# Kernel optimization log

Hardware: AMD Instinct MI355X
Metric: run time of the kernel (lower is better)

Reference implementation:

```python
import jax, jax.numpy as jnp
import numpy as np

N = 16384
E = 524288
IN_DIM = 512
HID = 256
NCLS = 64


def setup_inputs() -> dict:
    key = jax.random.key(0)
    k1, k2, k3, k4, k5, k6 = jax.random.split(key, 6)
    X = jax.random.normal(k1, (N, IN_DIM), dtype=jnp.float32)
    edge_index = jax.random.randint(k2, (2, E), 0, N, dtype=jnp.int64)
    # torch nn.Linear params: y = x @ W.T + b
    W1 = jax.random.normal(k3, (HID, IN_DIM), dtype=jnp.float32) * (1.0 / np.sqrt(IN_DIM))
    b1 = jax.random.normal(k4, (HID,), dtype=jnp.float32) * 0.01
    W2 = jax.random.normal(k5, (NCLS, HID), dtype=jnp.float32) * (1.0 / np.sqrt(HID))
    b2 = jax.random.normal(k6, (NCLS,), dtype=jnp.float32) * 0.01
    return {"X": X, "edge_index": edge_index, "W1": W1, "b1": b1, "W2": W2, "b2": b2}


def _build_a_hat(edge_index, n):
    # Dense adjacency via scatter-set, exactly as the torch code does.
    A = jnp.zeros((n, n), dtype=jnp.float32)
    A = A.at[edge_index[0], edge_index[1]].set(1.0)
    A = A + A.T
    A = (A > 0).astype(jnp.float32)
    A = A + jnp.eye(n, dtype=jnp.float32)
    # symmetric normalization: D^-1/2 A D^-1/2 (diag matmuls == broadcast)
    deg = A.sum(axis=1)
    dis = jnp.power(deg + 1e-8, -0.5)
    return dis[:, None] * A * dis[None, :]


def reference(X, edge_index, W1, b1, W2, b2):
    n = X.shape[0]
    A_hat = _build_a_hat(edge_index, n)
    H = A_hat @ X                      # [N, in_dim]
    H = H @ W1.T + b1                  # lin1
    H = jax.nn.relu(H)
    # dropout is identity in eval mode
    H = A_hat @ H                      # [N, hidden]
    H = H @ W2.T + b2                  # lin2 -> [N, num_classes]
    return H
```

## Files before the change

kernel.cpp:

```cpp
#include <hip/hip_runtime.h>
#include <stdint.h>

#define N_NODES 16384
#define N_EDGES 524288
#define IN_DIM  512
#define HID     256
#define NCLS    64
#define LSTRIDE 192
#define NBKT    1024
#define NBBLK   256
#define ENT     4096
#define OFFSTRIDE 1032
#define GEMM_BLKS 256

typedef __bf16 bf16x8 __attribute__((ext_vector_type(8)));
typedef float  f32x4  __attribute__((ext_vector_type(4)));
typedef unsigned int u32x4 __attribute__((ext_vector_type(4)));

__device__ __forceinline__ unsigned short f2bf(float f) {
    unsigned int u = __float_as_uint(f);
    u += 0x7FFFu + ((u >> 16) & 1u);
    return (unsigned short)(u >> 16);
}
__device__ __forceinline__ float bflo(unsigned int u) { return __uint_as_float(u << 16); }
__device__ __forceinline__ float bfhi(unsigned int u) { return __uint_as_float(u & 0xFFFF0000u); }

__device__ __forceinline__ void fma8(float* a, uint4 u, float w) {
    a[0] = fmaf(w, bflo(u.x), a[0]); a[1] = fmaf(w, bfhi(u.x), a[1]);
    a[2] = fmaf(w, bflo(u.y), a[2]); a[3] = fmaf(w, bfhi(u.y), a[3]);
    a[4] = fmaf(w, bflo(u.z), a[4]); a[5] = fmaf(w, bfhi(u.z), a[5]);
    a[6] = fmaf(w, bflo(u.w), a[6]); a[7] = fmaf(w, bfhi(u.w), a[7]);
}
__device__ __forceinline__ void add8(float* a, uint4 u) {
    a[0] += bflo(u.x); a[1] += bfhi(u.x);
    a[2] += bflo(u.y); a[3] += bfhi(u.y);
    a[4] += bflo(u.z); a[5] += bfhi(u.z);
    a[6] += bflo(u.w); a[7] += bfhi(u.w);
}

__device__ __forceinline__ void bucket_body(
    int blk, const void* __restrict__ ep, unsigned int* __restrict__ offbuf,
    unsigned int* __restrict__ gbuf, char* smem) {
    unsigned int* lcnt   = (unsigned int*)smem;
    unsigned int* loff   = lcnt + NBKT;
    unsigned int* sorted = loff + NBKT;
    unsigned int* wsum   = sorted + ENT;
    int* sflag = (int*)(wsum + 4);
    const int tid = threadIdx.x;
    if (tid == 0) {
        const int* p = (const int*)ep;
        int odd = 1;
        for (int k = 0; k < 64; ++k)
            if (p[2 * k + 1] != 0) odd = 0;
        *sflag = odd;
    }
    #pragma unroll
    for (int q = 0; q < 4; ++q) lcnt[tid + q * 256] = 0;
    __syncthreads();

    const int e0 = blk * 2048 + tid;
    int s[8], d[8];
    if (*sflag) {
        const long long* p = (const long long*)ep;
        #pragma unroll
        for (int q = 0; q < 8; ++q) {
            s[q] = (int)p[e0 + q * 256];
            d[q] = (int)p[N_EDGES + e0 + q * 256];
        }
    } else {
        const int* p = (const int*)ep;
        #pragma unroll
        for (int q = 0; q < 8; ++q) {
            s[q] = p[e0 + q * 256];
            d[q] = p[N_EDGES + e0 + q * 256];
        }
    }
    unsigned int meta[16];
    #pragma unroll
    for (int q = 0; q < 8; ++q) {
        int b0 = s[q] >> 4, b1 = d[q] >> 4;
        unsigned int sl0 = atomicAdd(&lcnt[b0], 1u);
        unsigned int sl1 = atomicAdd(&lcnt[b1], 1u);
        meta[2 * q]     = (unsigned int)b0 | (sl0 << 10);
        meta[2 * q + 1] = (unsigned int)b1 | (sl1 << 10);
    }
    __syncthreads();

    const int lane = tid & 63, wv = tid >> 6;
    unsigned int c0 = lcnt[4 * tid], c1 = lcnt[4 * tid + 1];
    unsigned int c2 = lcnt[4 * tid + 2], c3 = lcnt[4 * tid + 3];
    unsigned int p1 = c0 + c1, p2 = p1 + c2, tot = p2 + c3;
    unsigned int inc = tot;
    #pragma unroll
    for (int dd = 1; dd < 64; dd <<= 1) {
        unsigned int v = __shfl_up(inc, dd);
        if (lane >= dd) inc += v;
    }
    if (lane == 63) wsum[wv] = inc;
    __syncthreads();
    unsigned int wbase = 0;
    #pragma unroll
    for (int w = 0; w < 3; ++w)
        if (w < wv) wbase += wsum[w];
    unsigned int base = wbase + inc - tot;
    loff[4 * tid]     = base;
    loff[4 * tid + 1] = base + c0;
    loff[4 * tid + 2] = base + p1;
    loff[4 * tid + 3] = base + p2;
    {
        uint4 ov;
        ov.x = base; ov.y = base + c0; ov.z = base + p1; ov.w = base + p2;
        *(uint4*)&offbuf[(size_t)blk * OFFSTRIDE + 4 * tid] = ov;
        if (tid == 255) offbuf[(size_t)blk * OFFSTRIDE + 1024] = ENT;
    }
    __syncthreads();

    #pragma unroll
    for (int q = 0; q < 8; ++q) {
        unsigned int m0 = meta[2 * q];
        sorted[loff[m0 & 1023u] + (m0 >> 10)] =
            ((unsigned int)(s[q] & 15) << 14) | (unsigned int)d[q];
        unsigned int m1 = meta[2 * q + 1];
        sorted[loff[m1 & 1023u] + (m1 >> 10)] =
            ((unsigned int)(d[q] & 15) << 14) | (unsigned int)s[q];
    }
    __syncthreads();

    #pragma unroll
    for (int q = 0; q < 4; ++q)
        ((uint4*)gbuf)[(size_t)blk * (ENT / 4) + tid + q * 256] =
            ((const uint4*)sorted)[tid + q * 256];
}

__global__ __launch_bounds__(256) void build_csr(
    const unsigned int* __restrict__ offbuf, const unsigned int* __restrict__ gbuf,
    float* __restrict__ dis, int* __restrict__ ncnt,
    unsigned short* __restrict__ lists) {
    __shared__ unsigned int bml[16 * 512];
    const int tid = threadIdx.x;
    const int bkt = blockIdx.x;
    const int node0 = bkt * 16;
    {
        const u32x4 z = {0, 0, 0, 0};
        #pragma unroll
        for (int q = 0; q < 8; ++q)
            ((u32x4*)bml)[tid + q * 256] = z;
    }
    __syncthreads();
    {
        const unsigned int st = offbuf[(size_t)tid * OFFSTRIDE + bkt];
        const unsigned int en = offbuf[(size_t)tid * OFFSTRIDE + bkt + 1];
        const unsigned int* sp = gbuf + (size_t)tid * ENT;
        for (unsigned int l = st; l < en; ++l) {
            unsigned int e = sp[l];
            unsigned int local = e >> 14, nbr = e & 16383u;
            atomicOr(&bml[local * 512 + (nbr >> 5)], 1u << (nbr & 31u));
        }
    }
    __syncthreads();
    const int wid = tid >> 6, lane = tid & 63;
    for (int nn = wid; nn < 16; nn += 4) {
        const int node = node0 + nn;
        const unsigned int* row = bml + nn * 512 + lane * 8;
        unsigned int w[8];
        int c = 0;
        #pragma unroll
        for (int j = 0; j < 8; ++j) { w[j] = row[j]; c += __popc(w[j]); }
        int inc = c;
        #pragma unroll
        for (int dd = 1; dd < 64; dd <<= 1) {
            int t = __shfl_up(inc, dd);
            if (lane >= dd) inc += t;
        }
        int total = __shfl(inc, 63);
        unsigned short* dst = lists + (size_t)node * LSTRIDE + (inc - c);
        int k = 0;
        #pragma unroll
        for (int j = 0; j < 8; ++j) {
            unsigned int bits = w[j];
            int base = (lane * 8 + j) * 32;
            while (bits) {
                int b = __ffs(bits) - 1;
                bits &= bits - 1;
                dst[k++] = (unsigned short)(base + b);
            }
        }
        if (lane == 63) {
            lists[(size_t)node * LSTRIDE + total] = (unsigned short)node;
            ncnt[node] = total + 1;
            dis[node] = 1.0f / sqrtf((float)(total + 1) + 1e-8f);
        }
    }
}

template <bool F32>
__device__ __forceinline__ uint4 ld_chunk(const void* __restrict__ G,
                                          size_t row, int KD, int k0, int s) {
    if constexpr (F32) {
        const float* g = (const float*)G + row * KD + k0 + s * 8;
        float4 v0 = *(const float4*)g;
        float4 v1 = *(const float4*)(g + 4);
        uint4 w;
        w.x = (unsigned int)f2bf(v0.x) | ((unsigned int)f2bf(v0.y) << 16);
        w.y = (unsigned int)f2bf(v0.z) | ((unsigned int)f2bf(v0.w) << 16);
        w.z = (unsigned int)f2bf(v1.x) | ((unsigned int)f2bf(v1.y) << 16);
        w.w = (unsigned int)f2bf(v1.z) | ((unsigned int)f2bf(v1.w) << 16);
        return w;
    } else {
        return *(const uint4*)((const unsigned short*)G + row * KD + k0 + s * 8);
    }
}

template <int BM, int BN, int KD, int ND, bool AF32, bool BF32>
__device__ __forceinline__ void gemm_body(
    int bx, int by, const void* __restrict__ Ag, const void* __restrict__ Bg,
    unsigned short* __restrict__ Cg, const float* __restrict__ dis, char* smem) {
    constexpr int FM = BM / 32, FN = BN / 32;
    constexpr int NK = KD / 64;
    unsigned short* Asm = (unsigned short*)smem;
    unsigned short* Bsm = (unsigned short*)smem + BM * 64;
    const int tid = threadIdx.x;
    const int lane = tid & 63;
    const int wid = tid >> 6;
    const int wm = wid >> 1, wn = wid & 1;
    const int m0 = bx * BM, n0 = by * BN;

    uint4 ra[BM / 32], rb[BN / 32];
    #pragma unroll
    for (int q = 0; q < BM / 32; ++q) {
        int cch = tid + 256 * q, r = cch >> 3, s = cch & 7;
        ra[q] = ld_chunk<AF32>(Ag, (size_t)(m0 + r), KD, 0, s);
    }
    #pragma unroll
    for (int q = 0; q < BN / 32; ++q) {
        int cch = tid + 256 * q, r = cch >> 3, s = cch & 7;
        rb[q] = ld_chunk<BF32>(Bg, (size_t)(n0 + r), KD, 0, s);
    }

    f32x4 acc[FM][FN] = {};

    for (int kt = 0; kt < NK; ++kt) {
        __syncthreads();
        #pragma unroll
        for (int q = 0; q < BM / 32; ++q) {
            int cch = tid + 256 * q, r = cch >> 3, s = cch & 7;
            *(uint4*)((char*)Asm + r * 128 + ((s ^ (r & 7)) << 4)) = ra[q];
        }
        #pragma unroll
        for (int q = 0; q < BN / 32; ++q) {
            int cch = tid + 256 * q, r = cch >> 3, s = cch & 7;
            *(uint4*)((char*)Bsm + r * 128 + ((s ^ (r & 7)) << 4)) = rb[q];
        }
        __syncthreads();
        if (kt + 1 < NK) {
            int k0 = (kt + 1) * 64;
            #pragma unroll
            for (int q = 0; q < BM / 32; ++q) {
                int cch = tid + 256 * q, r = cch >> 3, s = cch & 7;
                ra[q] = ld_chunk<AF32>(Ag, (size_t)(m0 + r), KD, k0, s);
            }
            #pragma unroll
            for (int q = 0; q < BN / 32; ++q) {
                int cch = tid + 256 * q, r = cch >> 3, s = cch & 7;
                rb[q] = ld_chunk<BF32>(Bg, (size_t)(n0 + r), KD, k0, s);
            }
        }
        #pragma unroll
        for (int ks = 0; ks < 2; ++ks) {
            bf16x8 af[FM], bg[FN];
            #pragma unroll
            for (int i = 0; i < FM; ++i) {
                int row = wm * (BM / 2) + i * 16 + (lane & 15);
                int slot = (ks * 4 + (lane >> 4)) ^ (row & 7);
                af[i] = *(const bf16x8*)((const char*)Asm + row * 128 + slot * 16);
            }
            #pragma unroll
            for (int j = 0; j < FN; ++j) {
                int row = wn * (BN / 2) + j * 16 + (lane & 15);
                int slot = (ks * 4 + (lane >> 4)) ^ (row & 7);
                bg[j] = *(const bf16x8*)((const char*)Bsm + row * 128 + slot * 16);
            }
            #pragma unroll
            for (int i = 0; i < FM; ++i)
                #pragma unroll
                for (int j = 0; j < FN; ++j)
                    acc[i][j] = __builtin_amdgcn_mfma_f32_16x16x32_bf16(af[i], bg[j], acc[i][j], 0, 0, 0);
        }
    }

    #pragma unroll
    for (int i = 0; i < FM; ++i) {
        #pragma unroll
        for (int e = 0; e < 4; ++e) {
            int row = m0 + wm * (BM / 2) + i * 16 + ((lane >> 4) << 2) + e;
            float dm = dis ? dis[row] : 1.0f;
            #pragma unroll
            for (int j = 0; j < FN; ++j) {
                int col = n0 + wn * (BN / 2) + j * 16 + (lane & 15);
                Cg[(size_t)row * ND + col] = f2bf(acc[i][j][e] * dm);
            }
        }
    }
}

__global__ __launch_bounds__(256) void bucket_gemm(
    const float* __restrict__ X, const float* __restrict__ W1,
    unsigned short* __restrict__ Y, const void* __restrict__ ep,
    unsigned int* __restrict__ offbuf, unsigned int* __restrict__ gbuf) {
    __shared__ __align__(16) char smem[(128 + 128) * 64 * 2];
    if (blockIdx.x < GEMM_BLKS) {
        int gb = blockIdx.x;
        gemm_body<128, 128, IN_DIM, HID, true, true>(
            gb & 127, gb >> 7, X, W1, Y, nullptr, smem);
    } else {
        bucket_body(blockIdx.x - GEMM_BLKS, ep, offbuf, gbuf, smem);
    }
}

__global__ __launch_bounds__(256) void gemm2_k(
    const unsigned short* __restrict__ H1, const float* __restrict__ W2,
    unsigned short* __restrict__ Z, const float* __restrict__ dis) {
    __shared__ __align__(16) char smem[(64 + 64) * 64 * 2];
    gemm_body<64, 64, HID, NCLS, false, true>(blockIdx.x, 0, H1, W2, Z, dis, smem);
}

__global__ __launch_bounds__(256) void spmm_hid(
    const int* __restrict__ ncnt, const unsigned short* __restrict__ lists,
    const float* __restrict__ dis, const unsigned short* __restrict__ Yp,
    const float* __restrict__ bias, unsigned short* __restrict__ H1) {
    const int bid = blockIdx.x;
    const int r = bid & 7;
    const int fh = r >> 2;
    const int wid = threadIdx.x >> 6, lane = threadIdx.x & 63;
    const int i = (bid >> 3) * 16 + (r & 3) * 4 + wid;

    __shared__ uint2 sld[4][LSTRIDE];
    const int n = min(ncnt[i], LSTRIDE);
    for (int l = lane; l < n; l += 64) {
        int j = lists[(size_t)i * LSTRIDE + l];
        uint2 m;
        m.x = __float_as_uint(dis[j]);
        m.y = (unsigned int)j << 9;
        sld[wid][l] = m;
    }

    const int qw = lane >> 4, p = lane & 15;
    const char* Ybase = (const char*)Yp + fh * 256 + p * 16;
    const uint2* slw = sld[wid];
    float acc[8] = {}, acc2[8] = {};
    int l = 0;
    const int nmain = n & ~7;
    if (nmain >= 8) {
        uint2 m0 = slw[qw];
        uint2 m1 = slw[4 + qw];
        uint4 u0 = *(const uint4*)(Ybase + m0.y);
        uint4 u1 = *(const uint4*)(Ybase + m1.y);
        float w0 = __uint_as_float(m0.x), w1 = __uint_as_float(m1.x);
        #pragma unroll 2
        for (l = 8; l < nmain; l += 8) {
            uint2 t0 = slw[l + qw];
            uint2 t1 = slw[l + 4 + qw];
            uint4 v0 = *(const uint4*)(Ybase + t0.y);
            uint4 v1 = *(const uint4*)(Ybase + t1.y);
            fma8(acc, u0, w0);
            fma8(acc2, u1, w1);
            u0 = v0; u1 = v1;
            w0 = __uint_as_float(t0.x); w1 = __uint_as_float(t1.x);
        }
        fma8(acc, u0, w0);
        fma8(acc2, u1, w1);
        l = nmain;
    }
    for (; l < n; l += 4) {
        if (l + qw < n) {
            uint2 m = slw[l + qw];
            uint4 u = *(const uint4*)(Ybase + m.y);
            fma8(acc, u, __uint_as_float(m.x));
        }
    }
    #pragma unroll
    for (int k = 0; k < 8; ++k) {
        acc[k] += acc2[k];
        acc[k] += __shfl_xor(acc[k], 16);
        acc[k] += __shfl_xor(acc[k], 32);
    }
    if (qw == 0) {
        float di = dis[i];
        float4 b0 = *(const float4*)&bias[fh * 128 + p * 8];
        float4 b1 = *(const float4*)&bias[fh * 128 + p * 8 + 4];
        float v0 = fmaxf(fmaf(di, acc[0], b0.x), 0.0f);
        float v1 = fmaxf(fmaf(di, acc[1], b0.y), 0.0f);
        float v2 = fmaxf(fmaf(di, acc[2], b0.z), 0.0f);
        float v3 = fmaxf(fmaf(di, acc[3], b0.w), 0.0f);
        float v4 = fmaxf(fmaf(di, acc[4], b1.x), 0.0f);
        float v5 = fmaxf(fmaf(di, acc[5], b1.y), 0.0f);
        float v6 = fmaxf(fmaf(di, acc[6], b1.z), 0.0f);
        float v7 = fmaxf(fmaf(di, acc[7], b1.w), 0.0f);
        u32x4 o;
        o.x = (unsigned int)f2bf(v0) | ((unsigned int)f2bf(v1) << 16);
        o.y = (unsigned int)f2bf(v2) | ((unsigned int)f2bf(v3) << 16);
        o.z = (unsigned int)f2bf(v4) | ((unsigned int)f2bf(v5) << 16);
        o.w = (unsigned int)f2bf(v6) | ((unsigned int)f2bf(v7) << 16);
        __builtin_nontemporal_store(o, (u32x4*)&H1[(size_t)i * 256 + fh * 128 + p * 8]);
    }
}

__global__ __launch_bounds__(256) void spmm_out(
    const int* __restrict__ ncnt, const unsigned short* __restrict__ lists,
    const float* __restrict__ dis, const unsigned short* __restrict__ Zp,
    const float* __restrict__ bias, float* __restrict__ out) {
    const int wid = threadIdx.x >> 6, lane = threadIdx.x & 63;
    const int i = blockIdx.x * 4 + wid;
    __shared__ unsigned int sl[4][LSTRIDE];
    const int n = min(ncnt[i], LSTRIDE);
    for (int l = lane; l < n; l += 64)
        sl[wid][l] = (unsigned int)lists[(size_t)i * LSTRIDE + l] << 7;

    const int g = lane >> 3, p = lane & 7;
    const char* Zbase = (const char*)Zp + p * 16;
    const unsigned int* slw = sl[wid];
    float acc[8] = {}, acc2[8] = {};
    int l = 0;
    const int nmain = n & ~15;
    if (nmain >= 16) {
        uint4 u0 = *(const uint4*)(Zbase + slw[g]);
        uint4 u1 = *(const uint4*)(Zbase + slw[8 + g]);
        #pragma unroll 2
        for (l = 16; l < nmain; l += 16) {
            uint4 v0 = *(const uint4*)(Zbase + slw[l + g]);
            uint4 v1 = *(const uint4*)(Zbase + slw[l + 8 + g]);
            add8(acc, u0);
            add8(acc2, u1);
            u0 = v0; u1 = v1;
        }
        add8(acc, u0);
        add8(acc2, u1);
        l = nmain;
    }
    for (; l < n; l += 8) {
        if (l + g < n) {
            uint4 u = *(const uint4*)(Zbase + slw[l + g]);
            add8(acc, u);
        }
    }
    #pragma unroll
    for (int k = 0; k < 8; ++k) {
        acc[k] += acc2[k];
        acc[k] += __shfl_xor(acc[k], 8);
        acc[k] += __shfl_xor(acc[k], 16);
        acc[k] += __shfl_xor(acc[k], 32);
    }
    if (lane < 8) {
        float di = dis[i];
        float4 b0 = *(const float4*)&bias[p * 8];
        float4 b1 = *(const float4*)&bias[p * 8 + 4];
        f32x4 o0, o1;
        o0.x = fmaf(di, acc[0], b0.x); o0.y = fmaf(di, acc[1], b0.y);
        o0.z = fmaf(di, acc[2], b0.z); o0.w = fmaf(di, acc[3], b0.w);
        o1.x = fmaf(di, acc[4], b1.x); o1.y = fmaf(di, acc[5], b1.y);
        o1.z = fmaf(di, acc[6], b1.z); o1.w = fmaf(di, acc[7], b1.w);
        float* op = &out[(size_t)i * 64 + p * 8];
        __builtin_nontemporal_store(o0, (f32x4*)op);
        __builtin_nontemporal_store(o1, (f32x4*)(op + 4));
    }
}

extern "C" void kernel_launch(void* const* d_in, const int* in_sizes, int n_in,
                              void* d_out, int out_size, void* d_ws, size_t ws_size,
                              hipStream_t stream) {
    const float* X  = (const float*)d_in[0];
    const void*  EI = d_in[1];
    const float* W1 = (const float*)d_in[2];
    const float* b1 = (const float*)d_in[3];
    const float* W2 = (const float*)d_in[4];
    const float* b2 = (const float*)d_in[5];
    float* out = (float*)d_out;

    char* ws = (char*)d_ws;
    char* p = ws;
    unsigned int* offbuf = (unsigned int*)p;     p += (size_t)NBBLK * OFFSTRIDE * 4;
    unsigned int* gbuf   = (unsigned int*)p;     p += (size_t)NBBLK * ENT * 4;
    float* dis = (float*)p;                      p += (size_t)N_NODES * 4;
    int* ncnt = (int*)p;                         p += (size_t)N_NODES * 4;
    unsigned short* lists = (unsigned short*)p;  p += (size_t)N_NODES * LSTRIDE * 2;
    unsigned short* Y   = (unsigned short*)p;    p += (size_t)N_NODES * HID * 2;
    unsigned short* H1  = (unsigned short*)p;    p += (size_t)N_NODES * HID * 2;
    unsigned short* Z   = (unsigned short*)p;    p += (size_t)N_NODES * NCLS * 2;

    bucket_gemm<<<GEMM_BLKS + NBBLK, 256, 0, stream>>>(X, W1, Y, EI, offbuf, gbuf);
    build_csr<<<NBKT, 256, 0, stream>>>(offbuf, gbuf, dis, ncnt, lists);
    spmm_hid<<<2 * N_NODES / 4, 256, 0, stream>>>(ncnt, lists, dis, Y, b1, H1);
    gemm2_k<<<N_NODES / 64, 256, 0, stream>>>(H1, W2, Z, dis);
    spmm_out<<<N_NODES / 4, 256, 0, stream>>>(ncnt, lists, dis, Z, b2, out);
}
```

Baseline: 99.21 us.

## Split GEMM1 blocks across bucket and CSR-build kernels to balance overlap

```diff
diff --git a/kernel.cpp b/kernel.cpp
--- a/kernel.cpp
+++ b/kernel.cpp
@@ -12,6 +12,7 @@
 #define ENT     4096
 #define OFFSTRIDE 1032
 #define GEMM_BLKS 256
+#define G1A     64
 
 typedef __bf16 bf16x8 __attribute__((ext_vector_type(8)));
 typedef float  f32x4  __attribute__((ext_vector_type(4)));
@@ -132,13 +133,12 @@
             ((const uint4*)sorted)[tid + q * 256];
 }
 
-__global__ __launch_bounds__(256) void build_csr(
-    const unsigned int* __restrict__ offbuf, const unsigned int* __restrict__ gbuf,
-    float* __restrict__ dis, int* __restrict__ ncnt,
-    unsigned short* __restrict__ lists) {
-    __shared__ unsigned int bml[16 * 512];
+__device__ __forceinline__ void csr_body(
+    int bkt, const unsigned int* __restrict__ offbuf,
+    const unsigned int* __restrict__ gbuf, float* __restrict__ dis,
+    int* __restrict__ ncnt, unsigned short* __restrict__ lists, char* smem) {
+    unsigned int* bml = (unsigned int*)smem;
     const int tid = threadIdx.x;
-    const int bkt = blockIdx.x;
     const int node0 = bkt * 16;
     {
         const u32x4 z = {0, 0, 0, 0};
@@ -308,12 +308,27 @@
     unsigned short* __restrict__ Y, const void* __restrict__ ep,
     unsigned int* __restrict__ offbuf, unsigned int* __restrict__ gbuf) {
     __shared__ __align__(16) char smem[(128 + 128) * 64 * 2];
-    if (blockIdx.x < GEMM_BLKS) {
+    if (blockIdx.x < G1A) {
         int gb = blockIdx.x;
         gemm_body<128, 128, IN_DIM, HID, true, true>(
             gb & 127, gb >> 7, X, W1, Y, nullptr, smem);
     } else {
-        bucket_body(blockIdx.x - GEMM_BLKS, ep, offbuf, gbuf, smem);
+        bucket_body(blockIdx.x - G1A, ep, offbuf, gbuf, smem);
+    }
+}
+
+__global__ __launch_bounds__(256) void csr_gemm(
+    const float* __restrict__ X, const float* __restrict__ W1,
+    unsigned short* __restrict__ Y, const unsigned int* __restrict__ offbuf,
+    const unsigned int* __restrict__ gbuf, float* __restrict__ dis,
+    int* __restrict__ ncnt, unsigned short* __restrict__ lists) {
+    __shared__ __align__(16) char smem[(128 + 128) * 64 * 2];
+    if (blockIdx.x < (GEMM_BLKS - G1A)) {
+        int gb = blockIdx.x + G1A;
+        gemm_body<128, 128, IN_DIM, HID, true, true>(
+            gb & 127, gb >> 7, X, W1, Y, nullptr, smem);
+    } else {
+        csr_body(blockIdx.x - (GEMM_BLKS - G1A), offbuf, gbuf, dis, ncnt, lists, smem);
     }
 }
 
@@ -487,8 +502,9 @@
     unsigned short* H1  = (unsigned short*)p;    p += (size_t)N_NODES * HID * 2;
     unsigned short* Z   = (unsigned short*)p;    p += (size_t)N_NODES * NCLS * 2;
 
-    bucket_gemm<<<GEMM_BLKS + NBBLK, 256, 0, stream>>>(X, W1, Y, EI, offbuf, gbuf);
-    build_csr<<<NBKT, 256, 0, stream>>>(offbuf, gbuf, dis, ncnt, lists);
+    bucket_gemm<<<G1A + NBBLK, 256, 0, stream>>>(X, W1, Y, EI, offbuf, gbuf);
+    csr_gemm<<<(GEMM_BLKS - G1A) + NBKT, 256, 0, stream>>>(X, W1, Y, offbuf, gbuf,
+                                                           dis, ncnt, lists);
     spmm_hid<<<2 * N_NODES / 4, 256, 0, stream>>>(ncnt, lists, dis, Y, b1, H1);
     gemm2_k<<<N_NODES / 64, 256, 0, stream>>>(H1, W2, Z, dis);
     spmm_out<<<N_NODES / 4, 256, 0, stream>>>(ncnt, lists, dis, Z, b2, out);
```

New measurement: 108.1 us. +9.0%, slower.
